# Kernel optimization log

Hardware: AMD Instinct MI355X
Metric: run time of the kernel (lower is better)

## Reference

```python
import jax, jax.numpy as jnp
import numpy as np

TAU = 100.0
DT = 20.0
ALPHA = DT / TAU  # 0.2, fixed buffer (train_alpha=False)


def setup_inputs() -> dict:
    key = jax.random.key(0)
    ks = jax.random.split(key, 12)
    T, B, I, H = 64, 32, 128, 256

    def lin(kw, out_f, in_f):
        bound = 1.0 / np.sqrt(in_f)
        kw1, kw2 = jax.random.split(kw)
        w = jax.random.uniform(kw1, (out_f, in_f), jnp.float32, -bound, bound)
        b = jax.random.uniform(kw2, (out_f,), jnp.float32, -bound, bound)
        return w, b

    w_i2h, b_i2h = lin(ks[0], H, I)
    w_h2h, b_h2h = lin(ks[1], H, H)
    w_i2c, b_i2c = lin(ks[2], H, I)
    w_c2c, b_c2c = lin(ks[3], H, H)
    w_c2t, b_c2t = lin(ks[4], H * H, H)
    x = jax.random.normal(ks[5], (T, B, I), jnp.float32)
    return {
        "input": x,
        "w_i2h": w_i2h, "b_i2h": b_i2h,
        "w_h2h": w_h2h, "b_h2h": b_h2h,
        "w_i2c": w_i2c, "b_i2c": b_i2c,
        "w_c2c": w_c2c, "b_c2c": b_c2c,
        "w_c2t": w_c2t, "b_c2t": b_c2t,
        "num_steps": 1,
    }


def reference(input, w_i2h, b_i2h, w_h2h, b_h2h, w_i2c, b_i2c,
              w_c2c, b_c2c, w_c2t, b_c2t, num_steps):
    H = w_i2h.shape[0]
    B = input.shape[1]
    a = jnp.float32(ALPHA)

    def recurrence(x, hidden, context):
        input_proj = x @ w_i2h.T + b_i2h                      # [B,H]
        tm = (context @ w_c2t.T + b_c2t).reshape(B, H, H)     # per-sample hypernet matrix
        transformed = jnp.einsum('bij,bj->bi', tm, input_proj)
        h_new = jax.nn.relu(context + transformed + hidden @ w_h2h.T + b_h2h)
        hidden = hidden * (1 - a) + h_new * a
        context_new = jax.nn.relu(context @ w_c2c.T + b_c2c + x @ w_i2c.T + b_i2c)
        context = context * (1 - a) + context_new * a
        hidden = transformed  # NOTE: faithful to source, overwrites leaky update
        return hidden, context

    def step(carry, x):
        hidden, context = carry
        for _ in range(num_steps):
            hidden, context = recurrence(x, hidden, context)
        return (hidden, context), hidden

    h0 = jnp.zeros((B, H), input.dtype)
    c0 = jnp.zeros((B, H), input.dtype)
    (hidden, context), output = jax.lax.scan(step, (h0, c0), input)
    return output, hidden, context
```

## Files before the change

### kernel.cpp

```cpp
#include <hip/hip_runtime.h>

#define TT 64
#define BB 32
#define II 128
#define HH 256
#define MM (TT*BB)

typedef __bf16  bf16x8  __attribute__((ext_vector_type(8)));
typedef float   f32x16  __attribute__((ext_vector_type(16)));
typedef _Float16 half2v __attribute__((ext_vector_type(2)));
typedef unsigned int u32;

__device__ __forceinline__ float bf2f(unsigned short u) {
    union { unsigned int i; float f; } v; v.i = ((unsigned int)u) << 16; return v.f;
}
__device__ __forceinline__ unsigned short f2bf(float f) {
    union { float f; unsigned int i; } v; v.f = f;
    unsigned int r = v.i + 0x7fffu + ((v.i >> 16) & 1u);
    return (unsigned short)(r >> 16);
}

__device__ __forceinline__ void gload16(const unsigned short* g, unsigned short* l) {
    __builtin_amdgcn_global_load_lds(
        (const __attribute__((address_space(1))) u32*)g,
        (__attribute__((address_space(3))) u32*)l,
        16, 0, 0);
}

struct F8 { float v[8]; };
__device__ __forceinline__ F8 load8(const void* base, int idx, int isf32) {
    F8 r;
    if (isf32) {
        const float4* p = (const float4*)((const float*)base + idx);
        float4 a = p[0], b = p[1];
        r.v[0]=a.x; r.v[1]=a.y; r.v[2]=a.z; r.v[3]=a.w;
        r.v[4]=b.x; r.v[5]=b.y; r.v[6]=b.z; r.v[7]=b.w;
    } else {
        uint4 u = *(const uint4*)((const unsigned short*)base + idx);
        const unsigned short* p = (const unsigned short*)&u;
#pragma unroll
        for (int j = 0; j < 8; ++j) r.v[j] = bf2f(p[j]);
    }
    return r;
}
__device__ __forceinline__ float load1(const void* base, int idx, int isf32) {
    return isf32 ? ((const float*)base)[idx]
                 : bf2f(((const unsigned short*)base)[idx]);
}

__device__ __forceinline__ float fdot2f(half2v a, half2v b, float c) {
#if __has_builtin(__builtin_amdgcn_fdot2)
    return __builtin_amdgcn_fdot2(a, b, c, false);
#else
    return c + (float)a.x*(float)b.x + (float)a.y*(float)b.y;
#endif
}

__global__ __launch_bounds__(256) void k0_sniff(
    const unsigned short* __restrict__ x, int* __restrict__ flag)
{
    __shared__ int cnt;
    if (threadIdx.x == 0) cnt = 0;
    __syncthreads();
    int c = 0;
    for (int i = threadIdx.x; i < 8192; i += 256) {
        unsigned int e = (x[i] >> 7) & 0xFFu;
        if (e >= 0xC0u) ++c;
    }
    atomicAdd(&cnt, c);
    __syncthreads();
    if (threadIdx.x == 0) flag[0] = (cnt > 16) ? 1 : 0;
}

__global__ __launch_bounds__(256) void k1_proj(
    const void* __restrict__ x,
    const void* __restrict__ w_i2h,
    const void* __restrict__ b_i2h,
    const void* __restrict__ w_i2c,
    const void* __restrict__ b_i2c,
    const int* __restrict__ flagp,
    unsigned short* __restrict__ ipT,
    float* __restrict__ cin)
{
    const int isf32 = *flagp;
    const int tid = threadIdx.x;
    const int h = tid;
    const int mbase = blockIdx.x * 32;
    __shared__ __align__(16) _Float16 xs[32][II];
    __shared__ __align__(16) unsigned short ips[32][HH];

    half2v w1[II/2], w2[II/2];
#pragma unroll
    for (int c8 = 0; c8 < II/8; ++c8) {
        F8 f1 = load8(w_i2h, h*II + c8*8, isf32);
        F8 f2 = load8(w_i2c, h*II + c8*8, isf32);
#pragma unroll
        for (int j = 0; j < 4; ++j) {
            half2v a; a.x = (_Float16)f1.v[2*j]; a.y = (_Float16)f1.v[2*j+1];
            half2v b; b.x = (_Float16)f2.v[2*j]; b.y = (_Float16)f2.v[2*j+1];
            w1[c8*4 + j] = a;
            w2[c8*4 + j] = b;
        }
    }
    const float bb1 = load1(b_i2h, h, isf32);
    const float bb2 = load1(b_i2c, h, isf32);

    for (int u = tid; u < 32*II; u += 256)
        xs[u >> 7][u & (II-1)] = (_Float16)load1(x, (mbase + (u >> 7))*II + (u & (II-1)), isf32);
    __syncthreads();

    for (int mm = 0; mm < 32; ++mm) {
        const half2v* xv = (const half2v*)xs[mm];
        float a0=0,a1=0,a2=0,a3=0, c0=0,c1=0,c2=0,c3=0;
#pragma unroll
        for (int r = 0; r < II/2; r += 4) {
            half2v x0 = xv[r], x1 = xv[r+1], x2 = xv[r+2], x3 = xv[r+3];
            a0 = fdot2f(w1[r],   x0, a0);
            a1 = fdot2f(w1[r+1], x1, a1);
            a2 = fdot2f(w1[r+2], x2, a2);
            a3 = fdot2f(w1[r+3], x3, a3);
            c0 = fdot2f(w2[r],   x0, c0);
            c1 = fdot2f(w2[r+1], x1, c1);
            c2 = fdot2f(w2[r+2], x2, c2);
            c3 = fdot2f(w2[r+3], x3, c3);
        }
        ips[mm][h] = f2bf(((a0+a1)+(a2+a3)) + bb1);
        cin[(mbase+mm)*HH + h] = ((c0+c1)+(c2+c3)) + bb2;
    }
    __syncthreads();
    unsigned short tmp[32];
#pragma unroll
    for (int mm = 0; mm < 32; ++mm) tmp[mm] = ips[mm][tid];
    uint4* dst = (uint4*)(ipT + (size_t)tid*MM + mbase);
    const uint4* s4 = (const uint4*)tmp;
    dst[0] = s4[0]; dst[1] = s4[1]; dst[2] = s4[2]; dst[3] = s4[3];
}

__global__ __launch_bounds__(256) void k2_ctx(
    const void* __restrict__ w_c2c,
    const void* __restrict__ b_c2c,
    const float* __restrict__ cin,
    const int* __restrict__ ns_ptr,
    const int* __restrict__ flagp,
    unsigned short* __restrict__ ctx_hist,
    void* __restrict__ out_base)
{
    const int isf32 = *flagp;
    const int b = blockIdx.x;
    const int h = threadIdx.x;
    const int ns = max(1, *ns_ptr);

    __shared__ __align__(16) _Float16 cs[2][HH];

    half2v w[HH/2];
#pragma unroll
    for (int c8 = 0; c8 < HH/8; ++c8) {
        F8 f = load8(w_c2c, h*HH + c8*8, isf32);
#pragma unroll
        for (int j = 0; j < 4; ++j) {
            half2v hv;
            hv.x = (_Float16)f.v[2*j];
            hv.y = (_Float16)f.v[2*j+1];
            w[c8*4 + j] = hv;
        }
    }
    const float bcc = load1(b_c2c, h, isf32);
    float ctxv = 0.0f;
    cs[0][h] = (_Float16)0.0f;
    __syncthreads();
    int cur = 0;

    for (int t = 0; t < TT; ++t) {
        const float cinv = cin[(t*BB + b)*HH + h];
        for (int s = 0; s < ns; ++s) {
            if (s == ns-1) ctx_hist[(t*BB + b)*HH + h] = f2bf(ctxv);
            float p0=0,p1=0,p2=0,p3=0;
            const float4* cp4 = (const float4*)cs[cur];
#pragma unroll
            for (int r4 = 0; r4 < HH/8; ++r4) {
                float4 blob = cp4[r4];
                const half2v* c2 = (const half2v*)&blob;
                p0 = fdot2f(w[r4*4+0], c2[0], p0);
                p1 = fdot2f(w[r4*4+1], c2[1], p1);
                p2 = fdot2f(w[r4*4+2], c2[2], p2);
                p3 = fdot2f(w[r4*4+3], c2[3], p3);
            }
            float cnew = fmaxf(((p0+p1)+(p2+p3)) + bcc + cinv, 0.0f);
            ctxv = 0.8f*ctxv + 0.2f*cnew;
            cs[cur^1][h] = (_Float16)ctxv;
            cur ^= 1;
            __syncthreads();
        }
    }
    const int cofs = MM*HH + BB*HH + b*HH + h;
    if (isf32) ((float*)out_base)[cofs] = ctxv;
    else       ((unsigned short*)out_base)[cofs] = f2bf(ctxv);
}

__global__ __launch_bounds__(256) void k25_zero(float* __restrict__ outT)
{
    const int idx = (blockIdx.x * 256 + threadIdx.x) * 4;
    *(float4*)(outT + idx) = make_float4(0.f, 0.f, 0.f, 0.f);
}

__global__ __launch_bounds__(512, 2) void k3_main(
    const unsigned short* __restrict__ ctx_hist,
    const void* __restrict__ wc,
    const void* __restrict__ bc,
    const unsigned short* __restrict__ ipT,
    const int* __restrict__ flagp,
    float* __restrict__ outT)
{
    extern __shared__ __align__(16) unsigned char lds[];
    unsigned short* Ws   = (unsigned short*)lds;
    unsigned short* ring = (unsigned short*)(lds + 65536);
    float*          Ps   = (float*)(lds + 65536);

    const int isf32 = *flagp;
    const int tid  = threadIdx.x;
    const int lane = tid & 63;
    const int wave = tid >> 6;
    const int bx   = blockIdx.x;
    const int i    = bx >> 1;
    const int jh   = bx & 1;
    const int jq   = wave & 1;
    const int ms   = wave >> 1;
    const int l31  = lane & 31;
    const int lhi  = lane >> 5;

#pragma unroll
    for (int p = 0; p < 8; ++p) {
        const int u = tid + p*512;
        const int jrow = u >> 5, cu = u & 31;
        F8 f = load8(wc, (i*HH + jh*128 + jrow)*HH + cu*8, isf32);
        unsigned short tmp[8];
#pragma unroll
        for (int j = 0; j < 8; ++j) tmp[j] = f2bf(f.v[j]);
        *(uint4*)(Ws + (cu*128 + jrow)*8) = *(const uint4*)tmp;
    }
    asm volatile("s_waitcnt lgkmcnt(0)" ::: "memory");

    const int u0 = wave*128 + lane;
    const int m0row = u0 & 255, k0u = u0 >> 8;
    const int u1 = u0 + 64;
    const int m1row = u1 & 255, k1u = u1 >> 8;
    const int wb0 = (wave*128)*8;
    const int wb1 = (wave*128 + 64)*8;

    const int wbase = (jq*64 + l31)*8;
    const int bofs  = (lhi*256 + ms*64 + l31)*8;

#pragma unroll 1
    for (int mc = 0; mc < 8; ++mc) {
        const unsigned short* gm = ctx_hist + (size_t)(mc*256)*HH;

        f32x16 acc[2][2];
#pragma unroll
        for (int a = 0; a < 2; ++a)
#pragma unroll
            for (int g = 0; g < 4; ++g) {
                const int jb = i*HH + jh*128 + jq*64 + a*32 + g*8 + lhi*4;
                float b0, b1, b2, b3;
                if (isf32) {
                    float4 t = *(const float4*)((const float*)bc + jb);
                    b0 = t.x; b1 = t.y; b2 = t.z; b3 = t.w;
                } else {
                    ushort4 t = *(const ushort4*)((const unsigned short*)bc + jb);
                    b0 = bf2f(t.x); b1 = bf2f(t.y); b2 = bf2f(t.z); b3 = bf2f(t.w);
                }
                acc[a][0][g*4+0] = b0; acc[a][1][g*4+0] = b0;
                acc[a][0][g*4+1] = b1; acc[a][1][g*4+1] = b1;
                acc[a][0][g*4+2] = b2; acc[a][1][g*4+2] = b2;
                acc[a][0][g*4+3] = b3; acc[a][1][g*4+3] = b3;
            }

#pragma unroll
        for (int c = 0; c < 3; ++c) {
            gload16(gm + m0row*HH + c*32 + k0u*8, ring + c*8192 + wb0);
            gload16(gm + m1row*HH + c*32 + k1u*8, ring + c*8192 + wb1);
        }

#pragma unroll
        for (int kc = 0; kc < 8; ++kc) {
            if (kc < 6)       asm volatile("s_waitcnt vmcnt(4)" ::: "memory");
            else if (kc == 6) asm volatile("s_waitcnt vmcnt(2)" ::: "memory");
            else              asm volatile("s_waitcnt vmcnt(0)" ::: "memory");
            __builtin_amdgcn_s_barrier();
            if (kc < 5) {
                const int c = kc + 3, rb = c & 3;
                gload16(gm + m0row*HH + c*32 + k0u*8, ring + rb*8192 + wb0);
                gload16(gm + m1row*HH + c*32 + k1u*8, ring + rb*8192 + wb1);
            }
            const unsigned short* Ac = ring + (kc & 3)*8192;
#pragma unroll
            for (int ks = 0; ks < 2; ++ks) {
                const int ku = kc*4 + ks*2 + lhi;
                bf16x8 w0 = *(const bf16x8*)(Ws + ku*1024 + wbase);
                bf16x8 w1 = *(const bf16x8*)(Ws + ku*1024 + wbase + 256);
                bf16x8 b0 = *(const bf16x8*)(Ac + bofs + ks*4096);
                bf16x8 b1 = *(const bf16x8*)(Ac + bofs + ks*4096 + 256);
                __builtin_amdgcn_s_setprio(1);
                acc[0][0] = __builtin_amdgcn_mfma_f32_32x32x16_bf16(w0, b0, acc[0][0], 0, 0, 0);
                acc[0][1] = __builtin_amdgcn_mfma_f32_32x32x16_bf16(w0, b1, acc[0][1], 0, 0, 0);
                acc[1][0] = __builtin_amdgcn_mfma_f32_32x32x16_bf16(w1, b0, acc[1][0], 0, 0, 0);
                acc[1][1] = __builtin_amdgcn_mfma_f32_32x32x16_bf16(w1, b1, acc[1][1], 0, 0, 0);
                __builtin_amdgcn_s_setprio(0);
            }
        }

        float sv0 = 0.0f, sv1 = 0.0f;
        const int mcol = mc*256 + ms*64 + l31;
#pragma unroll
        for (int a = 0; a < 2; ++a)
#pragma unroll
            for (int g = 0; g < 4; ++g) {
                const unsigned short* prow =
                    ipT + (jh*128 + jq*64 + a*32 + g*8 + lhi*4)*MM + mcol;
#pragma unroll
                for (int q = 0; q < 4; ++q) {
                    sv0 = fmaf(acc[a][0][g*4+q], bf2f(prow[q*MM]),      sv0);
                    sv1 = fmaf(acc[a][1][g*4+q], bf2f(prow[q*MM + 32]), sv1);
                }
            }
        sv0 += __shfl_xor(sv0, 32);
        sv1 += __shfl_xor(sv1, 32);
        if (lhi == 0) {
            Ps[jq*256 + ms*64 +      l31] = sv0;
            Ps[jq*256 + ms*64 + 32 + l31] = sv1;
        }
        __syncthreads();
        if (tid < 256)
            atomicAdd(&outT[(size_t)i*MM + mc*256 + tid], Ps[tid] + Ps[256+tid]);
        __syncthreads();
    }
}

__global__ __launch_bounds__(256) void k4_tr(
    const float* __restrict__ outT,
    const int* __restrict__ flagp,
    void* __restrict__ out)
{
    const int isf32 = *flagp;
    __shared__ float tile[64][65];
    const int t  = threadIdx.x;
    const int bm = blockIdx.x * 64;
    const int bi = blockIdx.y * 64;
#pragma unroll
    for (int p = 0; p < 16; ++p) {
        const int u = t + p*256;
        const int r = u >> 6, c = u & 63;
        tile[r][c] = outT[(size_t)(bi + r)*MM + bm + c];
    }
    __syncthreads();
#pragma unroll
    for (int p = 0; p < 16; ++p) {
        const int u = t + p*256;
        const int r = u >> 6, c = u & 63;
        const float v = tile[c][r];
        const int m = bm + r;
        if (isf32) {
            float* o = (float*)out;
            o[(size_t)m*HH + bi + c] = v;
            if (m >= MM - BB) o[(size_t)MM*HH + (m - (MM-BB))*HH + bi + c] = v;
        } else {
            unsigned short* o = (unsigned short*)out;
            const unsigned short vb = f2bf(v);
            o[(size_t)m*HH + bi + c] = vb;
            if (m >= MM - BB) o[(size_t)MM*HH + (m - (MM-BB))*HH + bi + c] = vb;
        }
    }
}

extern "C" void kernel_launch(void* const* d_in, const int* in_sizes, int n_in,
                              void* d_out, int out_size, void* d_ws, size_t ws_size,
                              hipStream_t stream) {
    const void* x     = d_in[0];
    const void* w_i2h = d_in[1];
    const void* b_i2h = d_in[2];
    const void* w_i2c = d_in[5];
    const void* b_i2c = d_in[6];
    const void* w_c2c = d_in[7];
    const void* b_c2c = d_in[8];
    const void* w_c2t = d_in[9];
    const void* b_c2t = d_in[10];
    const int* ns     = (const int*)d_in[11];

    unsigned short* ipT = (unsigned short*)d_ws;
    unsigned short* ch  = (unsigned short*)((char*)d_ws + (size_t)MM*HH*2);
    float* cin          = (float*)((char*)d_ws + (size_t)MM*HH*4);
    float* outT         = cin;
    int* flag           = (int*)((char*)d_ws + (size_t)MM*HH*8);

    (void)hipFuncSetAttribute((const void*)k3_main,
                              hipFuncAttributeMaxDynamicSharedMemorySize, 131072);

    k0_sniff<<<1, 256, 0, stream>>>((const unsigned short*)x, flag);
    k1_proj<<<64, 256, 0, stream>>>(x, w_i2h, b_i2h, w_i2c, b_i2c, flag, ipT, cin);
    k2_ctx<<<BB, 256, 0, stream>>>(w_c2c, b_c2c, cin, ns, flag, ch, d_out);
    k25_zero<<<512, 256, 0, stream>>>(outT);
    k3_main<<<512, 512, 131072, stream>>>(ch, w_c2t, b_c2t, ipT, flag, outT);
    k4_tr<<<dim3(32, 4), 256, 0, stream>>>(outT, flag, d_out);
}
```

Measured before the change: 332.4 us.

## Double M-tile per block to 512 rows with 3-stage ring buffer

```diff
diff --git a/kernel.cpp b/kernel.cpp
--- a/kernel.cpp
+++ b/kernel.cpp
@@ -240,21 +240,17 @@
     }
     asm volatile("s_waitcnt lgkmcnt(0)" ::: "memory");
 
-    const int u0 = wave*128 + lane;
-    const int m0row = u0 & 255, k0u = u0 >> 8;
-    const int u1 = u0 + 64;
-    const int m1row = u1 & 255, k1u = u1 >> 8;
-    const int wb0 = (wave*128)*8;
-    const int wb1 = (wave*128 + 64)*8;
+    const unsigned short* gbase = ctx_hist + (size_t)tid*HH;
+    const int wu = (tid & ~63)*8;
 
     const int wbase = (jq*64 + l31)*8;
-    const int bofs  = (lhi*256 + ms*64 + l31)*8;
+    const int bofs  = (ms*128 + l31)*8;
 
 #pragma unroll 1
-    for (int mc = 0; mc < 8; ++mc) {
-        const unsigned short* gm = ctx_hist + (size_t)(mc*256)*HH;
-
-        f32x16 acc[2][2];
+    for (int mc = 0; mc < 4; ++mc) {
+        const unsigned short* gm = gbase + (size_t)(mc*512)*HH;
+
+        f32x16 acc[2][4];
 #pragma unroll
         for (int a = 0; a < 2; ++a)
 #pragma unroll
@@ -268,69 +264,81 @@
                     ushort4 t = *(const ushort4*)((const unsigned short*)bc + jb);
                     b0 = bf2f(t.x); b1 = bf2f(t.y); b2 = bf2f(t.z); b3 = bf2f(t.w);
                 }
-                acc[a][0][g*4+0] = b0; acc[a][1][g*4+0] = b0;
-                acc[a][0][g*4+1] = b1; acc[a][1][g*4+1] = b1;
-                acc[a][0][g*4+2] = b2; acc[a][1][g*4+2] = b2;
-                acc[a][0][g*4+3] = b3; acc[a][1][g*4+3] = b3;
+#pragma unroll
+                for (int n = 0; n < 4; ++n) {
+                    acc[a][n][g*4+0] = b0;
+                    acc[a][n][g*4+1] = b1;
+                    acc[a][n][g*4+2] = b2;
+                    acc[a][n][g*4+3] = b3;
+                }
             }
 
 #pragma unroll
-        for (int c = 0; c < 3; ++c) {
-            gload16(gm + m0row*HH + c*32 + k0u*8, ring + c*8192 + wb0);
-            gload16(gm + m1row*HH + c*32 + k1u*8, ring + c*8192 + wb1);
-        }
+        for (int c = 0; c < 2; ++c)
+#pragma unroll
+            for (int p = 0; p < 4; ++p)
+                gload16(gm + c*32 + p*8, ring + c*16384 + p*4096 + wu);
 
 #pragma unroll
         for (int kc = 0; kc < 8; ++kc) {
-            if (kc < 6)       asm volatile("s_waitcnt vmcnt(4)" ::: "memory");
-            else if (kc == 6) asm volatile("s_waitcnt vmcnt(2)" ::: "memory");
-            else              asm volatile("s_waitcnt vmcnt(0)" ::: "memory");
+            if (kc < 7) asm volatile("s_waitcnt vmcnt(4)" ::: "memory");
+            else        asm volatile("s_waitcnt vmcnt(0)" ::: "memory");
             __builtin_amdgcn_s_barrier();
-            if (kc < 5) {
-                const int c = kc + 3, rb = c & 3;
-                gload16(gm + m0row*HH + c*32 + k0u*8, ring + rb*8192 + wb0);
-                gload16(gm + m1row*HH + c*32 + k1u*8, ring + rb*8192 + wb1);
+            if (kc < 6) {
+                const int c = kc + 2, rb = c % 3;
+#pragma unroll
+                for (int p = 0; p < 4; ++p)
+                    gload16(gm + c*32 + p*8, ring + rb*16384 + p*4096 + wu);
             }
-            const unsigned short* Ac = ring + (kc & 3)*8192;
+            const unsigned short* Ac = ring + (kc % 3)*16384;
 #pragma unroll
             for (int ks = 0; ks < 2; ++ks) {
-                const int ku = kc*4 + ks*2 + lhi;
-                bf16x8 w0 = *(const bf16x8*)(Ws + ku*1024 + wbase);
-                bf16x8 w1 = *(const bf16x8*)(Ws + ku*1024 + wbase + 256);
-                bf16x8 b0 = *(const bf16x8*)(Ac + bofs + ks*4096);
-                bf16x8 b1 = *(const bf16x8*)(Ac + bofs + ks*4096 + 256);
+                const int kuW = kc*4 + ks*2 + lhi;
+                const int kuL = ks*2 + lhi;
+                bf16x8 w0 = *(const bf16x8*)(Ws + kuW*1024 + wbase);
+                bf16x8 w1 = *(const bf16x8*)(Ws + kuW*1024 + wbase + 256);
+                bf16x8 b0 = *(const bf16x8*)(Ac + kuL*4096 + bofs);
+                bf16x8 b1 = *(const bf16x8*)(Ac + kuL*4096 + bofs + 256);
+                bf16x8 b2 = *(const bf16x8*)(Ac + kuL*4096 + bofs + 512);
+                bf16x8 b3 = *(const bf16x8*)(Ac + kuL*4096 + bofs + 768);
                 __builtin_amdgcn_s_setprio(1);
                 acc[0][0] = __builtin_amdgcn_mfma_f32_32x32x16_bf16(w0, b0, acc[0][0], 0, 0, 0);
                 acc[0][1] = __builtin_amdgcn_mfma_f32_32x32x16_bf16(w0, b1, acc[0][1], 0, 0, 0);
+                acc[0][2] = __builtin_amdgcn_mfma_f32_32x32x16_bf16(w0, b2, acc[0][2], 0, 0, 0);
+                acc[0][3] = __builtin_amdgcn_mfma_f32_32x32x16_bf16(w0, b3, acc[0][3], 0, 0, 0);
                 acc[1][0] = __builtin_amdgcn_mfma_f32_32x32x16_bf16(w1, b0, acc[1][0], 0, 0, 0);
                 acc[1][1] = __builtin_amdgcn_mfma_f32_32x32x16_bf16(w1, b1, acc[1][1], 0, 0, 0);
+                acc[1][2] = __builtin_amdgcn_mfma_f32_32x32x16_bf16(w1, b2, acc[1][2], 0, 0, 0);
+                acc[1][3] = __builtin_amdgcn_mfma_f32_32x32x16_bf16(w1, b3, acc[1][3], 0, 0, 0);
                 __builtin_amdgcn_s_setprio(0);
             }
         }
 
-        float sv0 = 0.0f, sv1 = 0.0f;
-        const int mcol = mc*256 + ms*64 + l31;
-#pragma unroll
-        for (int a = 0; a < 2; ++a)
-#pragma unroll
-            for (int g = 0; g < 4; ++g) {
-                const unsigned short* prow =
-                    ipT + (jh*128 + jq*64 + a*32 + g*8 + lhi*4)*MM + mcol;
-#pragma unroll
-                for (int q = 0; q < 4; ++q) {
-                    sv0 = fmaf(acc[a][0][g*4+q], bf2f(prow[q*MM]),      sv0);
-                    sv1 = fmaf(acc[a][1][g*4+q], bf2f(prow[q*MM + 32]), sv1);
+        const unsigned short* pb =
+            ipT + (size_t)(jh*128 + jq*64 + lhi*4)*MM + (mc*512 + ms*128 + l31);
+        float sv[4];
+#pragma unroll
+        for (int n = 0; n < 4; ++n) {
+            float s = 0.0f;
+#pragma unroll
+            for (int a = 0; a < 2; ++a)
+#pragma unroll
+                for (int g = 0; g < 4; ++g) {
+                    const unsigned short* prow = pb + (size_t)(a*32 + g*8)*MM + n*32;
+#pragma unroll
+                    for (int q = 0; q < 4; ++q)
+                        s = fmaf(acc[a][n][g*4+q], bf2f(prow[(size_t)q*MM]), s);
                 }
-            }
-        sv0 += __shfl_xor(sv0, 32);
-        sv1 += __shfl_xor(sv1, 32);
+            s += __shfl_xor(s, 32);
+            sv[n] = s;
+        }
         if (lhi == 0) {
-            Ps[jq*256 + ms*64 +      l31] = sv0;
-            Ps[jq*256 + ms*64 + 32 + l31] = sv1;
+#pragma unroll
+            for (int n = 0; n < 4; ++n)
+                Ps[jq*512 + ms*128 + n*32 + l31] = sv[n];
         }
         __syncthreads();
-        if (tid < 256)
-            atomicAdd(&outT[(size_t)i*MM + mc*256 + tid], Ps[tid] + Ps[256+tid]);
+        atomicAdd(&outT[(size_t)i*MM + mc*512 + tid], Ps[tid] + Ps[512+tid]);
         __syncthreads();
     }
 }
@@ -392,12 +400,12 @@
     int* flag           = (int*)((char*)d_ws + (size_t)MM*HH*8);
 
     (void)hipFuncSetAttribute((const void*)k3_main,
-                              hipFuncAttributeMaxDynamicSharedMemorySize, 131072);
+                              hipFuncAttributeMaxDynamicSharedMemorySize, 163840);
 
     k0_sniff<<<1, 256, 0, stream>>>((const unsigned short*)x, flag);
     k1_proj<<<64, 256, 0, stream>>>(x, w_i2h, b_i2h, w_i2c, b_i2c, flag, ipT, cin);
     k2_ctx<<<BB, 256, 0, stream>>>(w_c2c, b_c2c, cin, ns, flag, ch, d_out);
     k25_zero<<<512, 256, 0, stream>>>(outT);
-    k3_main<<<512, 512, 131072, stream>>>(ch, w_c2t, b_c2t, ipT, flag, outT);
+    k3_main<<<512, 512, 163840, stream>>>(ch, w_c2t, b_c2t, ipT, flag, outT);
     k4_tr<<<dim3(32, 4), 256, 0, stream>>>(outT, flag, d_out);
 }
```

Result: slower. 360.7 us (+8.5%).
